# Optimization experiments

Hardware: AMD Instinct MI355X
Metric: run time of the kernel (lower is better)

## Reference

```python
import jax, jax.numpy as jnp
import numpy as np

GAMMA = 0.5          # blending coeff from __init__
NEG_SLOPE = 0.2      # LeakyReLU slope
MASK_FILL = -9e15    # zero_vec constant from source

N, M, D = 8192, 8192, 256
SPARSITY = 0.01


def setup_inputs() -> dict:
    key = jax.random.key(0)
    k1, k2, k3, k4, k5 = jax.random.split(key, 5)
    input1 = jax.random.normal(k1, (N, D), dtype=jnp.float32)
    input2 = jax.random.normal(k2, (M, D), dtype=jnp.float32)
    adj = (jax.random.uniform(k3, (N, M)) < SPARSITY).astype(jnp.float32)
    # xavier_normal with gain=1.414 on (D,1): std = gain*sqrt(2/(D+1))
    std = 1.414 * np.sqrt(2.0 / (D + 1))
    a1 = jax.random.normal(k4, (D, 1), dtype=jnp.float32) * std
    a2 = jax.random.normal(k5, (D, 1), dtype=jnp.float32) * std
    return {"input1": input1, "input2": input2, "adj": adj, "a1": a1, "a2": a2}


def reference(input1, input2, adj, a1, a2):
    # e1: (N,1) broadcast against e2: (1,M) -> e: (N,M)
    e1 = input1 @ a1                      # (N,1)
    e2 = (input2 @ a2).T                  # (1,M)
    e = jax.nn.leaky_relu(e1 + e2, negative_slope=NEG_SLOPE)
    attention = jnp.where(adj > 0, e, MASK_FILL)
    attention = jax.nn.softmax(attention, axis=1)
    # scale each row by its adjacency degree, then gamma-blend with adj
    attention = attention * jnp.sum(adj, axis=1, keepdims=True)
    attention = attention * GAMMA + adj * (1.0 - GAMMA)
    return attention @ input2             # (N,D)
```

## Files before the change

### kernel.cpp

```cpp
#include <hip/hip_runtime.h>
#include <cstdint>
#include <cstddef>

#define NEG_SLOPE 0.2f
#define CAP 192
#define NB 4
#define RPB 16

typedef float f32x4 __attribute__((ext_vector_type(4)));
typedef unsigned short u16x4 __attribute__((ext_vector_type(4)));

static __device__ __forceinline__ unsigned short f2bf_rne(float f) {
  unsigned u = __float_as_uint(f);
  unsigned r = (u + 0x7FFFu + ((u >> 16) & 1u)) >> 16;
  return (unsigned short)r;
}
static __device__ __forceinline__ float bf2f(unsigned short h) {
  return __uint_as_float((unsigned)h << 16);
}

__global__ __launch_bounds__(256) void score_conv_kernel(
    const float* __restrict__ x1, const float* __restrict__ x2,
    const float* __restrict__ a1, const float* __restrict__ a2,
    float* __restrict__ e1, float* __restrict__ f2,
    unsigned short* __restrict__ x2h, int N, int M, int D) {
  int gtid = blockIdx.x * blockDim.x + threadIdx.x;
  int wid = gtid >> 6;
  int lane = threadIdx.x & 63;
  if (wid >= N + M) return;
  const float4 av = *reinterpret_cast<const float4*>(
      ((wid < N) ? a1 : a2) + lane * 4);
  if (wid < N) {
    const float4 xv = *reinterpret_cast<const float4*>(x1 + (size_t)wid * D + lane * 4);
    float s = xv.x * av.x + xv.y * av.y + xv.z * av.z + xv.w * av.w;
    #pragma unroll
    for (int off = 32; off > 0; off >>= 1) s += __shfl_down(s, off, 64);
    if (lane == 0) e1[wid] = s;
  } else {
    int row = wid - N;
    const float4 xv = *reinterpret_cast<const float4*>(x2 + (size_t)row * D + lane * 4);
    float s = xv.x * av.x + xv.y * av.y + xv.z * av.z + xv.w * av.w;
    u16x4 h;
    h.x = f2bf_rne(xv.x); h.y = f2bf_rne(xv.y);
    h.z = f2bf_rne(xv.z); h.w = f2bf_rne(xv.w);
    reinterpret_cast<u16x4*>(x2h)[(size_t)row * (D >> 2) + lane] = h;
    #pragma unroll
    for (int off = 32; off > 0; off >>= 1) s += __shfl_down(s, off, 64);
    if (lane == 0) f2[row] = s;
  }
}

__global__ __launch_bounds__(512) void attn_pc_kernel(
    const float* __restrict__ adj, const unsigned short* __restrict__ x2h,
    const float* __restrict__ e1, const float* __restrict__ f2,
    float* __restrict__ out, int N, int M, int D) {
  __shared__ float s_f2[8192];
  __shared__ int   s_idx[2][4][CAP];
  __shared__ float s_w[2][4][CAP];
  __shared__ int   s_cnt[2][4];

  const int tid  = threadIdx.x;
  const int wv   = tid >> 6;
  const int lane = tid & 63;
  const int D4   = D >> 2;

  {
    const f32x4* src = reinterpret_cast<const f32x4*>(f2);
    f32x4* dst = reinterpret_cast<f32x4*>(s_f2);
    #pragma unroll
    for (int i = 0; i < 4; ++i) dst[tid + i * 512] = src[tid + i * 512];
  }
  __syncthreads();

  const int base = blockIdx.x * RPB;
  const u16x4* __restrict__ x2h4 = reinterpret_cast<const u16x4*>(x2h);
  float4* __restrict__ out4 = reinterpret_cast<float4*>(out);

  for (int r = 0; r <= NB; ++r) {
    if (wv < 4) {
      if (r < NB) {
        const int row = base + r * 4 + wv;
        const int p = r & 1;
        if (row < N) {
          const float e1i = e1[row];
          const f32x4* __restrict__ arow4 =
              reinterpret_cast<const f32x4*>(adj + (size_t)row * M);
          uint64_t m0 = 0ull, m1 = 0ull;
          #pragma unroll 8
          for (int it = 0; it < 16; ++it) {
            f32x4 v = __builtin_nontemporal_load(&arow4[it * 64 + lane]);
            uint64_t b = 0;
            if (v.x > 0.f) b |= 1ull;
            if (v.y > 0.f) b |= 2ull;
            if (v.z > 0.f) b |= 4ull;
            if (v.w > 0.f) b |= 8ull;
            m0 |= b << (it * 4);
          }
          #pragma unroll 8
          for (int it = 16; it < 32; ++it) {
            f32x4 v = __builtin_nontemporal_load(&arow4[it * 64 + lane]);
            uint64_t b = 0;
            if (v.x > 0.f) b |= 1ull;
            if (v.y > 0.f) b |= 2ull;
            if (v.z > 0.f) b |= 4ull;
            if (v.w > 0.f) b |= 8ull;
            m1 |= b << ((it - 16) * 4);
          }
          const int cnt = __popcll(m0) + __popcll(m1);
          int incl = cnt;
          #pragma unroll
          for (int off = 1; off < 64; off <<= 1) {
            int t = __shfl_up(incl, off, 64);
            if (lane >= off) incl += t;
          }
          int pos = incl - cnt;
          const int K = __shfl(incl, 63, 64);

          while (m0) {
            int b = __ffsll((unsigned long long)m0) - 1;
            m0 &= m0 - 1;
            int j = ((((b >> 2) << 6) + lane) << 2) + (b & 3);
            float e = e1i + s_f2[j];
            e = (e > 0.f) ? e : NEG_SLOPE * e;
            if (pos < CAP) { s_idx[p][wv][pos] = j; s_w[p][wv][pos] = e; }
            ++pos;
          }
          while (m1) {
            int b = __ffsll((unsigned long long)m1) - 1;
            m1 &= m1 - 1;
            int j = (((((b >> 2) + 16) << 6) + lane) << 2) + (b & 3);
            float e = e1i + s_f2[j];
            e = (e > 0.f) ? e : NEG_SLOPE * e;
            if (pos < CAP) { s_idx[p][wv][pos] = j; s_w[p][wv][pos] = e; }
            ++pos;
          }

          const int Kc = (K < CAP) ? K : CAP;
          if (lane == 0) s_cnt[p][wv] = Kc;
          if (K > 0) {
            float lm = -1e30f;
            for (int k = lane; k < Kc; k += 64) lm = fmaxf(lm, s_w[p][wv][k]);
            #pragma unroll
            for (int off = 32; off > 0; off >>= 1)
              lm = fmaxf(lm, __shfl_xor(lm, off, 64));
            float ls = 0.f;
            for (int k = lane; k < Kc; k += 64) {
              float pr = __expf(s_w[p][wv][k] - lm);
              s_w[p][wv][k] = pr;
              ls += pr;
            }
            #pragma unroll
            for (int off = 32; off > 0; off >>= 1) ls += __shfl_xor(ls, off, 64);
            const float scale = 0.5f * (float)K / ls;
            for (int k = lane; k < Kc; k += 64)
              s_w[p][wv][k] = s_w[p][wv][k] * scale + 0.5f;
          }
        }
      }
    } else {
      if (r >= 1) {
        const int cw = wv - 4;
        const int row = base + (r - 1) * 4 + cw;
        const int p = (r - 1) & 1;
        if (row < N) {
          const int K = s_cnt[p][cw];
          if (K == 0) {
            float4 z; z.x = z.y = z.z = z.w = 0.f;
            out4[(size_t)row * D4 + lane] = z;
          } else {
            float4 a0, a1v, a2v, a3;
            a0.x = a0.y = a0.z = a0.w = 0.f; a1v = a0; a2v = a0; a3 = a0;
            int k = 0;
            for (; k + 4 <= K; k += 4) {
              int j0 = __builtin_amdgcn_readfirstlane(s_idx[p][cw][k + 0]);
              int j1 = __builtin_amdgcn_readfirstlane(s_idx[p][cw][k + 1]);
              int j2 = __builtin_amdgcn_readfirstlane(s_idx[p][cw][k + 2]);
              int j3 = __builtin_amdgcn_readfirstlane(s_idx[p][cw][k + 3]);
              float w0 = s_w[p][cw][k + 0], w1 = s_w[p][cw][k + 1];
              float w2 = s_w[p][cw][k + 2], w3 = s_w[p][cw][k + 3];
              u16x4 h0 = x2h4[(size_t)j0 * D4 + lane];
              u16x4 h1 = x2h4[(size_t)j1 * D4 + lane];
              u16x4 h2 = x2h4[(size_t)j2 * D4 + lane];
              u16x4 h3 = x2h4[(size_t)j3 * D4 + lane];
              a0.x = fmaf(w0, bf2f(h0.x), a0.x); a0.y = fmaf(w0, bf2f(h0.y), a0.y);
              a0.z = fmaf(w0, bf2f(h0.z), a0.z); a0.w = fmaf(w0, bf2f(h0.w), a0.w);
              a1v.x = fmaf(w1, bf2f(h1.x), a1v.x); a1v.y = fmaf(w1, bf2f(h1.y), a1v.y);
              a1v.z = fmaf(w1, bf2f(h1.z), a1v.z); a1v.w = fmaf(w1, bf2f(h1.w), a1v.w);
              a2v.x = fmaf(w2, bf2f(h2.x), a2v.x); a2v.y = fmaf(w2, bf2f(h2.y), a2v.y);
              a2v.z = fmaf(w2, bf2f(h2.z), a2v.z); a2v.w = fmaf(w2, bf2f(h2.w), a2v.w);
              a3.x = fmaf(w3, bf2f(h3.x), a3.x); a3.y = fmaf(w3, bf2f(h3.y), a3.y);
              a3.z = fmaf(w3, bf2f(h3.z), a3.z); a3.w = fmaf(w3, bf2f(h3.w), a3.w);
            }
            for (; k < K; ++k) {
              int j = __builtin_amdgcn_readfirstlane(s_idx[p][cw][k]);
              float w = s_w[p][cw][k];
              u16x4 h = x2h4[(size_t)j * D4 + lane];
              a0.x = fmaf(w, bf2f(h.x), a0.x); a0.y = fmaf(w, bf2f(h.y), a0.y);
              a0.z = fmaf(w, bf2f(h.z), a0.z); a0.w = fmaf(w, bf2f(h.w), a0.w);
            }
            float4 rr;
            rr.x = (a0.x + a1v.x) + (a2v.x + a3.x);
            rr.y = (a0.y + a1v.y) + (a2v.y + a3.y);
            rr.z = (a0.z + a1v.z) + (a2v.z + a3.z);
            rr.w = (a0.w + a1v.w) + (a2v.w + a3.w);
            out4[(size_t)row * D4 + lane] = rr;
          }
        }
      }
    }
    __syncthreads();
  }
}

extern "C" void kernel_launch(void* const* d_in, const int* in_sizes, int n_in,
                              void* d_out, int out_size, void* d_ws, size_t ws_size,
                              hipStream_t stream) {
  const float* x1  = (const float*)d_in[0];
  const float* x2  = (const float*)d_in[1];
  const float* adj = (const float*)d_in[2];
  const float* a1  = (const float*)d_in[3];
  const float* a2  = (const float*)d_in[4];
  float* out = (float*)d_out;

  const int D = in_sizes[3];
  const int N = in_sizes[0] / D;
  const int M = in_sizes[1] / D;

  char* p = (char*)d_ws;
  float* e1 = (float*)p;                    p += (size_t)N * 4;
  float* f2 = (float*)p;                    p += (size_t)M * 4;
  unsigned short* x2h = (unsigned short*)p;

  const int waves = N + M;
  const int blocks1 = (waves * 64 + 255) / 256;
  score_conv_kernel<<<blocks1, 256, 0, stream>>>(x1, x2, a1, a2, e1, f2, x2h, N, M, D);
  attn_pc_kernel<<<(N + RPB - 1) / RPB, 512, 0, stream>>>(adj, x2h, e1, f2, out, N, M, D);
}
```

Measured before the change: 89.52 us.

## Replace producer/consumer waves with per-wave register-prefetched row pipeline

The kernel drops the split where 4 producer waves built sparse lists and 4 consumer waves gathered, with a block barrier between stages. Each wave now owns 4 consecutive rows. It prefetches the next adjacency row into 32 vector registers while it processes the current row's softmax and gather, so the block-wide __syncthreads per stage goes away. Blocks shrink to 256 threads with occupancy hint 2 and CAP drops to 160. The 128-float register buffer raises VGPR pressure and may limit occupancy or cause spills. The lower CAP leaves less headroom for rows with many edges.

```diff
diff --git a/kernel.cpp b/kernel.cpp
--- a/kernel.cpp
+++ b/kernel.cpp
@@ -3,9 +3,8 @@
 #include <cstddef>
 
 #define NEG_SLOPE 0.2f
-#define CAP 192
-#define NB 4
-#define RPB 16
+#define CAP 160
+#define RPW 4
 
 typedef float f32x4 __attribute__((ext_vector_type(4)));
 typedef unsigned short u16x4 __attribute__((ext_vector_type(4)));
@@ -50,14 +49,13 @@
   }
 }
 
-__global__ __launch_bounds__(512) void attn_pc_kernel(
+__global__ __launch_bounds__(256, 2) void attn_pipe_kernel(
     const float* __restrict__ adj, const unsigned short* __restrict__ x2h,
     const float* __restrict__ e1, const float* __restrict__ f2,
     float* __restrict__ out, int N, int M, int D) {
   __shared__ float s_f2[8192];
-  __shared__ int   s_idx[2][4][CAP];
-  __shared__ float s_w[2][4][CAP];
-  __shared__ int   s_cnt[2][4];
+  __shared__ int   s_idx[4][CAP];
+  __shared__ float s_w[4][CAP];
 
   const int tid  = threadIdx.x;
   const int wv   = tid >> 6;
@@ -68,147 +66,148 @@
     const f32x4* src = reinterpret_cast<const f32x4*>(f2);
     f32x4* dst = reinterpret_cast<f32x4*>(s_f2);
     #pragma unroll
-    for (int i = 0; i < 4; ++i) dst[tid + i * 512] = src[tid + i * 512];
+    for (int i = 0; i < 8; ++i) dst[tid + i * 256] = src[tid + i * 256];
   }
   __syncthreads();
 
-  const int base = blockIdx.x * RPB;
+  const int rowbase = (blockIdx.x * 4 + wv) * RPW;
+  if (rowbase >= N) return;
+  const float4 e1v = *reinterpret_cast<const float4*>(e1 + rowbase);
+  const float e1s[4] = {e1v.x, e1v.y, e1v.z, e1v.w};
+
   const u16x4* __restrict__ x2h4 = reinterpret_cast<const u16x4*>(x2h);
   float4* __restrict__ out4 = reinterpret_cast<float4*>(out);
 
-  for (int r = 0; r <= NB; ++r) {
-    if (wv < 4) {
-      if (r < NB) {
-        const int row = base + r * 4 + wv;
-        const int p = r & 1;
-        if (row < N) {
-          const float e1i = e1[row];
-          const f32x4* __restrict__ arow4 =
-              reinterpret_cast<const f32x4*>(adj + (size_t)row * M);
-          uint64_t m0 = 0ull, m1 = 0ull;
-          #pragma unroll 8
-          for (int it = 0; it < 16; ++it) {
-            f32x4 v = __builtin_nontemporal_load(&arow4[it * 64 + lane]);
-            uint64_t b = 0;
-            if (v.x > 0.f) b |= 1ull;
-            if (v.y > 0.f) b |= 2ull;
-            if (v.z > 0.f) b |= 4ull;
-            if (v.w > 0.f) b |= 8ull;
-            m0 |= b << (it * 4);
-          }
-          #pragma unroll 8
-          for (int it = 16; it < 32; ++it) {
-            f32x4 v = __builtin_nontemporal_load(&arow4[it * 64 + lane]);
-            uint64_t b = 0;
-            if (v.x > 0.f) b |= 1ull;
-            if (v.y > 0.f) b |= 2ull;
-            if (v.z > 0.f) b |= 4ull;
-            if (v.w > 0.f) b |= 8ull;
-            m1 |= b << ((it - 16) * 4);
-          }
-          const int cnt = __popcll(m0) + __popcll(m1);
-          int incl = cnt;
-          #pragma unroll
-          for (int off = 1; off < 64; off <<= 1) {
-            int t = __shfl_up(incl, off, 64);
-            if (lane >= off) incl += t;
-          }
-          int pos = incl - cnt;
-          const int K = __shfl(incl, 63, 64);
-
-          while (m0) {
-            int b = __ffsll((unsigned long long)m0) - 1;
-            m0 &= m0 - 1;
-            int j = ((((b >> 2) << 6) + lane) << 2) + (b & 3);
-            float e = e1i + s_f2[j];
-            e = (e > 0.f) ? e : NEG_SLOPE * e;
-            if (pos < CAP) { s_idx[p][wv][pos] = j; s_w[p][wv][pos] = e; }
-            ++pos;
-          }
-          while (m1) {
-            int b = __ffsll((unsigned long long)m1) - 1;
-            m1 &= m1 - 1;
-            int j = (((((b >> 2) + 16) << 6) + lane) << 2) + (b & 3);
-            float e = e1i + s_f2[j];
-            e = (e > 0.f) ? e : NEG_SLOPE * e;
-            if (pos < CAP) { s_idx[p][wv][pos] = j; s_w[p][wv][pos] = e; }
-            ++pos;
-          }
-
-          const int Kc = (K < CAP) ? K : CAP;
-          if (lane == 0) s_cnt[p][wv] = Kc;
-          if (K > 0) {
-            float lm = -1e30f;
-            for (int k = lane; k < Kc; k += 64) lm = fmaxf(lm, s_w[p][wv][k]);
-            #pragma unroll
-            for (int off = 32; off > 0; off >>= 1)
-              lm = fmaxf(lm, __shfl_xor(lm, off, 64));
-            float ls = 0.f;
-            for (int k = lane; k < Kc; k += 64) {
-              float pr = __expf(s_w[p][wv][k] - lm);
-              s_w[p][wv][k] = pr;
-              ls += pr;
-            }
-            #pragma unroll
-            for (int off = 32; off > 0; off >>= 1) ls += __shfl_xor(ls, off, 64);
-            const float scale = 0.5f * (float)K / ls;
-            for (int k = lane; k < Kc; k += 64)
-              s_w[p][wv][k] = s_w[p][wv][k] * scale + 0.5f;
-          }
+  f32x4 hold[32];
+  {
+    const f32x4* ar = reinterpret_cast<const f32x4*>(adj + (size_t)rowbase * M) + lane;
+    #pragma unroll
+    for (int it = 0; it < 32; ++it) hold[it] = __builtin_nontemporal_load(ar + it * 64);
+  }
+
+  #pragma unroll
+  for (int r = 0; r < RPW; ++r) {
+    const int row = rowbase + r;
+    uint64_t m0 = 0ull, m1 = 0ull;
+    #pragma unroll
+    for (int it = 0; it < 16; ++it) {
+      f32x4 v = hold[it];
+      uint64_t b = 0;
+      if (v.x > 0.f) b |= 1ull;
+      if (v.y > 0.f) b |= 2ull;
+      if (v.z > 0.f) b |= 4ull;
+      if (v.w > 0.f) b |= 8ull;
+      m0 |= b << (it * 4);
+    }
+    #pragma unroll
+    for (int it = 16; it < 32; ++it) {
+      f32x4 v = hold[it];
+      uint64_t b = 0;
+      if (v.x > 0.f) b |= 1ull;
+      if (v.y > 0.f) b |= 2ull;
+      if (v.z > 0.f) b |= 4ull;
+      if (v.w > 0.f) b |= 8ull;
+      m1 |= b << ((it - 16) * 4);
+    }
+    if (r + 1 < RPW) {
+      const f32x4* nr =
+          reinterpret_cast<const f32x4*>(adj + (size_t)(row + 1) * M) + lane;
+      #pragma unroll
+      for (int it = 0; it < 32; ++it) hold[it] = __builtin_nontemporal_load(nr + it * 64);
+    }
+    __builtin_amdgcn_sched_barrier(0);
+
+    const float e1i = e1s[r];
+    const int cnt = __popcll(m0) + __popcll(m1);
+    int incl = cnt;
+    #pragma unroll
+    for (int off = 1; off < 64; off <<= 1) {
+      int t = __shfl_up(incl, off, 64);
+      if (lane >= off) incl += t;
+    }
+    int pos = incl - cnt;
+    const int K = __shfl(incl, 63, 64);
+
+    while (m0) {
+      int b = __ffsll((unsigned long long)m0) - 1;
+      m0 &= m0 - 1;
+      int j = ((((b >> 2) << 6) + lane) << 2) + (b & 3);
+      float e = e1i + s_f2[j];
+      e = (e > 0.f) ? e : NEG_SLOPE * e;
+      if (pos < CAP) { s_idx[wv][pos] = j; s_w[wv][pos] = e; }
+      ++pos;
+    }
+    while (m1) {
+      int b = __ffsll((unsigned long long)m1) - 1;
+      m1 &= m1 - 1;
+      int j = (((((b >> 2) + 16) << 6) + lane) << 2) + (b & 3);
+      float e = e1i + s_f2[j];
+      e = (e > 0.f) ? e : NEG_SLOPE * e;
+      if (pos < CAP) { s_idx[wv][pos] = j; s_w[wv][pos] = e; }
+      ++pos;
+    }
+
+    if (row < N) {
+      if (K == 0) {
+        float4 z; z.x = z.y = z.z = z.w = 0.f;
+        out4[(size_t)row * D4 + lane] = z;
+      } else {
+        const int Kc = (K < CAP) ? K : CAP;
+        float lm = -1e30f;
+        for (int k = lane; k < Kc; k += 64) lm = fmaxf(lm, s_w[wv][k]);
+        #pragma unroll
+        for (int off = 32; off > 0; off >>= 1)
+          lm = fmaxf(lm, __shfl_xor(lm, off, 64));
+        float ls = 0.f;
+        for (int k = lane; k < Kc; k += 64) {
+          float pr = __expf(s_w[wv][k] - lm);
+          s_w[wv][k] = pr;
+          ls += pr;
         }
+        #pragma unroll
+        for (int off = 32; off > 0; off >>= 1) ls += __shfl_xor(ls, off, 64);
+        const float scale = 0.5f * (float)K / ls;
+        for (int k = lane; k < Kc; k += 64)
+          s_w[wv][k] = s_w[wv][k] * scale + 0.5f;
+
+        float4 a0, a1v, a2v, a3;
+        a0.x = a0.y = a0.z = a0.w = 0.f; a1v = a0; a2v = a0; a3 = a0;
+        int k = 0;
+        for (; k + 4 <= Kc; k += 4) {
+          int j0 = __builtin_amdgcn_readfirstlane(s_idx[wv][k + 0]);
+          int j1 = __builtin_amdgcn_readfirstlane(s_idx[wv][k + 1]);
+          int j2 = __builtin_amdgcn_readfirstlane(s_idx[wv][k + 2]);
+          int j3 = __builtin_amdgcn_readfirstlane(s_idx[wv][k + 3]);
+          float w0 = s_w[wv][k + 0], w1 = s_w[wv][k + 1];
+          float w2 = s_w[wv][k + 2], w3 = s_w[wv][k + 3];
+          u16x4 h0 = x2h4[(size_t)j0 * D4 + lane];
+          u16x4 h1 = x2h4[(size_t)j1 * D4 + lane];
+          u16x4 h2 = x2h4[(size_t)j2 * D4 + lane];
+          u16x4 h3 = x2h4[(size_t)j3 * D4 + lane];
+          a0.x = fmaf(w0, bf2f(h0.x), a0.x); a0.y = fmaf(w0, bf2f(h0.y), a0.y);
+          a0.z = fmaf(w0, bf2f(h0.z), a0.z); a0.w = fmaf(w0, bf2f(h0.w), a0.w);
+          a1v.x = fmaf(w1, bf2f(h1.x), a1v.x); a1v.y = fmaf(w1, bf2f(h1.y), a1v.y);
+          a1v.z = fmaf(w1, bf2f(h1.z), a1v.z); a1v.w = fmaf(w1, bf2f(h1.w), a1v.w);
+          a2v.x = fmaf(w2, bf2f(h2.x), a2v.x); a2v.y = fmaf(w2, bf2f(h2.y), a2v.y);
+          a2v.z = fmaf(w2, bf2f(h2.z), a2v.z); a2v.w = fmaf(w2, bf2f(h2.w), a2v.w);
+          a3.x = fmaf(w3, bf2f(h3.x), a3.x); a3.y = fmaf(w3, bf2f(h3.y), a3.y);
+          a3.z = fmaf(w3, bf2f(h3.z), a3.z); a3.w = fmaf(w3, bf2f(h3.w), a3.w);
+        }
+        for (; k < Kc; ++k) {
+          int j = __builtin_amdgcn_readfirstlane(s_idx[wv][k]);
+          float w = s_w[wv][k];
+          u16x4 h = x2h4[(size_t)j * D4 + lane];
+          a0.x = fmaf(w, bf2f(h.x), a0.x); a0.y = fmaf(w, bf2f(h.y), a0.y);
+          a0.z = fmaf(w, bf2f(h.z), a0.z); a0.w = fmaf(w, bf2f(h.w), a0.w);
+        }
+        float4 rr;
+        rr.x = (a0.x + a1v.x) + (a2v.x + a3.x);
+        rr.y = (a0.y + a1v.y) + (a2v.y + a3.y);
+        rr.z = (a0.z + a1v.z) + (a2v.z + a3.z);
+        rr.w = (a0.w + a1v.w) + (a2v.w + a3.w);
+        out4[(size_t)row * D4 + lane] = rr;
       }
-    } else {
-      if (r >= 1) {
-        const int cw = wv - 4;
-        const int row = base + (r - 1) * 4 + cw;
-        const int p = (r - 1) & 1;
-        if (row < N) {
-          const int K = s_cnt[p][cw];
-          if (K == 0) {
-            float4 z; z.x = z.y = z.z = z.w = 0.f;
-            out4[(size_t)row * D4 + lane] = z;
-          } else {
-            float4 a0, a1v, a2v, a3;
-            a0.x = a0.y = a0.z = a0.w = 0.f; a1v = a0; a2v = a0; a3 = a0;
-            int k = 0;
-            for (; k + 4 <= K; k += 4) {
-              int j0 = __builtin_amdgcn_readfirstlane(s_idx[p][cw][k + 0]);
-              int j1 = __builtin_amdgcn_readfirstlane(s_idx[p][cw][k + 1]);
-              int j2 = __builtin_amdgcn_readfirstlane(s_idx[p][cw][k + 2]);
-              int j3 = __builtin_amdgcn_readfirstlane(s_idx[p][cw][k + 3]);
-              float w0 = s_w[p][cw][k + 0], w1 = s_w[p][cw][k + 1];
-              float w2 = s_w[p][cw][k + 2], w3 = s_w[p][cw][k + 3];
-              u16x4 h0 = x2h4[(size_t)j0 * D4 + lane];
-              u16x4 h1 = x2h4[(size_t)j1 * D4 + lane];
-              u16x4 h2 = x2h4[(size_t)j2 * D4 + lane];
-              u16x4 h3 = x2h4[(size_t)j3 * D4 + lane];
-              a0.x = fmaf(w0, bf2f(h0.x), a0.x); a0.y = fmaf(w0, bf2f(h0.y), a0.y);
-              a0.z = fmaf(w0, bf2f(h0.z), a0.z); a0.w = fmaf(w0, bf2f(h0.w), a0.w);
-              a1v.x = fmaf(w1, bf2f(h1.x), a1v.x); a1v.y = fmaf(w1, bf2f(h1.y), a1v.y);
-              a1v.z = fmaf(w1, bf2f(h1.z), a1v.z); a1v.w = fmaf(w1, bf2f(h1.w), a1v.w);
-              a2v.x = fmaf(w2, bf2f(h2.x), a2v.x); a2v.y = fmaf(w2, bf2f(h2.y), a2v.y);
-              a2v.z = fmaf(w2, bf2f(h2.z), a2v.z); a2v.w = fmaf(w2, bf2f(h2.w), a2v.w);
-              a3.x = fmaf(w3, bf2f(h3.x), a3.x); a3.y = fmaf(w3, bf2f(h3.y), a3.y);
-              a3.z = fmaf(w3, bf2f(h3.z), a3.z); a3.w = fmaf(w3, bf2f(h3.w), a3.w);
-            }
-            for (; k < K; ++k) {
-              int j = __builtin_amdgcn_readfirstlane(s_idx[p][cw][k]);
-              float w = s_w[p][cw][k];
-              u16x4 h = x2h4[(size_t)j * D4 + lane];
-              a0.x = fmaf(w, bf2f(h.x), a0.x); a0.y = fmaf(w, bf2f(h.y), a0.y);
-              a0.z = fmaf(w, bf2f(h.z), a0.z); a0.w = fmaf(w, bf2f(h.w), a0.w);
-            }
-            float4 rr;
-            rr.x = (a0.x + a1v.x) + (a2v.x + a3.x);
-            rr.y = (a0.y + a1v.y) + (a2v.y + a3.y);
-            rr.z = (a0.z + a1v.z) + (a2v.z + a3.z);
-            rr.w = (a0.w + a1v.w) + (a2v.w + a3.w);
-            out4[(size_t)row * D4 + lane] = rr;
-          }
-        }
-      }
-    }
-    __syncthreads();
+    }
   }
 }
 
@@ -234,5 +233,8 @@
   const int waves = N + M;
   const int blocks1 = (waves * 64 + 255) / 256;
   score_conv_kernel<<<blocks1, 256, 0, stream>>>(x1, x2, a1, a2, e1, f2, x2h, N, M, D);
-  attn_pc_kernel<<<(N + RPB - 1) / RPB, 512, 0, stream>>>(adj, x2h, e1, f2, out, N, M, D);
-}
+
+  const int rows_per_block = 4 * RPW;
+  attn_pipe_kernel<<<(N + rows_per_block - 1) / rows_per_block, 256, 0, stream>>>(
+      adj, x2h, e1, f2, out, N, M, D);
+}
```

Measured after the change: 94.10 us. +5.1%, slower.
